# Optimization experiments

Measured on AMD Instinct MI355X. Metric: run time of the kernel, lower is better.

Reference implementation:

```python
import jax, jax.numpy as jnp
import numpy as np

N_NODES = 100000
N_GRAPHS = 64
NEG_SLOPE = 0.2  # PyG GATConv default leaky_relu slope


def gat_conv(x, src, dst, W, a_src, a_dst, b, heads, out_c, concat, num_nodes):
    # x: [N, F_in]; W: [heads*out_c, F_in]; a_src/a_dst: [heads, out_c]
    h = (x @ W.T).reshape(num_nodes, heads, out_c)            # [N, H, C]
    s_src = jnp.sum(h * a_src, axis=-1)                       # [N, H]
    s_dst = jnp.sum(h * a_dst, axis=-1)                       # [N, H]
    e = jax.nn.leaky_relu(s_src[src] + s_dst[dst], NEG_SLOPE)  # [E, H]
    # segment softmax over incoming edges of each destination node
    m = jax.ops.segment_max(e, dst, num_segments=num_nodes)   # [N, H]
    m = jnp.where(jnp.isfinite(m), m, 0.0)
    e = jnp.exp(e - m[dst])
    denom = jax.ops.segment_sum(e, dst, num_segments=num_nodes)  # [N, H]
    alpha = e / (denom[dst] + 1e-16)                           # [E, H]
    msg = alpha[:, :, None] * h[src]                           # [E, H, C]
    out = jax.ops.segment_sum(msg, dst, num_segments=num_nodes)  # [N, H, C]
    if concat:
        out = out.reshape(num_nodes, heads * out_c)
    else:
        out = out.mean(axis=1)
    return out + b


def setup_inputs() -> dict:
    key = jax.random.key(0)
    ks = jax.random.split(key, 12)
    x = jax.random.normal(ks[0], (N_NODES, 128), dtype=jnp.float32)
    edge_index = jax.random.randint(ks[1], (2, 1600000), 0, N_NODES, dtype=jnp.int64)
    batch = jnp.sort(jax.random.randint(ks[2], (N_NODES,), 0, N_GRAPHS, dtype=jnp.int64))
    # conv1: 128 -> 16, heads=4, concat -> 64
    W1 = jax.random.normal(ks[3], (64, 128), dtype=jnp.float32) * 0.1
    att_src1 = jax.random.normal(ks[4], (4, 16), dtype=jnp.float32) * 0.1
    att_dst1 = jax.random.normal(ks[5], (4, 16), dtype=jnp.float32) * 0.1
    b1 = jnp.zeros((64,), dtype=jnp.float32)
    # conv2: 64 -> 10, heads=1, concat=False
    W2 = jax.random.normal(ks[6], (10, 64), dtype=jnp.float32) * 0.1
    att_src2 = jax.random.normal(ks[7], (1, 10), dtype=jnp.float32) * 0.1
    att_dst2 = jax.random.normal(ks[8], (1, 10), dtype=jnp.float32) * 0.1
    b2 = jnp.zeros((10,), dtype=jnp.float32)
    return {"x": x, "edge_index": edge_index, "batch": batch,
            "W1": W1, "att_src1": att_src1, "att_dst1": att_dst1, "b1": b1,
            "W2": W2, "att_src2": att_src2, "att_dst2": att_dst2, "b2": b2}


def reference(x, edge_index, batch, W1, att_src1, att_dst1, b1, W2, att_src2, att_dst2, b2):
    N = x.shape[0]
    # PyG GATConv adds self-loops by default
    loop = jnp.arange(N, dtype=edge_index.dtype)
    src = jnp.concatenate([edge_index[0], loop])
    dst = jnp.concatenate([edge_index[1], loop])
    # dropout layers are inactive in eval mode
    h = gat_conv(x, src, dst, W1, att_src1, att_dst1, b1, heads=4, out_c=16, concat=True, num_nodes=N)
    h = jax.nn.elu(h)
    h = gat_conv(h, src, dst, W2, att_src2, att_dst2, b2, heads=1, out_c=10, concat=False, num_nodes=N)
    # global_mean_pool over graphs in the batch
    sums = jax.ops.segment_sum(h, batch, num_segments=N_GRAPHS)
    counts = jax.ops.segment_sum(jnp.ones((N,), dtype=h.dtype), batch, num_segments=N_GRAPHS)
    pooled = sums / jnp.maximum(counts, 1.0)[:, None]
    return jax.nn.log_softmax(pooled, axis=1)
```

## Files before the change

kernel.cpp:

```cpp
#include <hip/hip_runtime.h>
#include <hip/hip_bf16.h>
#include <math.h>

#define BSHIFT 7
#define BWIDTH (1 << BSHIFT)
#define BCAP 2560
#define A3_TILE 4096

typedef float floatx2 __attribute__((ext_vector_type(2)));
typedef __attribute__((ext_vector_type(8))) short bf16x8;
typedef __attribute__((ext_vector_type(4))) float f32x4;

__device__ inline unsigned int f2bf(float f) {
    unsigned int u = __float_as_uint(f);
    return (u + 0x7FFFu + ((u >> 16) & 1u)) >> 16;
}
__device__ inline float bflo(unsigned int u) { return __uint_as_float(u << 16); }
__device__ inline float bfhi(unsigned int u) { return __uint_as_float(u & 0xFFFF0000u); }

__device__ inline void fp8x16_fma2(uint4 Wv, float we, floatx2* q) {
    floatx2 w2; w2[0] = we; w2[1] = we;
    q[0] += w2 * __builtin_amdgcn_cvt_pk_f32_fp8((int)Wv.x, false);
    q[1] += w2 * __builtin_amdgcn_cvt_pk_f32_fp8((int)Wv.x, true);
    q[2] += w2 * __builtin_amdgcn_cvt_pk_f32_fp8((int)Wv.y, false);
    q[3] += w2 * __builtin_amdgcn_cvt_pk_f32_fp8((int)Wv.y, true);
    q[4] += w2 * __builtin_amdgcn_cvt_pk_f32_fp8((int)Wv.z, false);
    q[5] += w2 * __builtin_amdgcn_cvt_pk_f32_fp8((int)Wv.z, true);
    q[6] += w2 * __builtin_amdgcn_cvt_pk_f32_fp8((int)Wv.w, false);
    q[7] += w2 * __builtin_amdgcn_cvt_pk_f32_fp8((int)Wv.w, true);
}

#define G1_BM 128

__device__ void gemm1_body(char* smem, int bid,
    const float* __restrict__ x, const float* __restrict__ W1,
    const float* __restrict__ a_src, const float* __restrict__ a_dst,
    unsigned char* __restrict__ h1f, float* __restrict__ s1s,
    float* __restrict__ s1d, int N)
{
    unsigned short (*xb)[136] = (unsigned short(*)[136])smem;
    unsigned short (*wb)[136] = (unsigned short(*)[136])(smem + 34816);
    float (*hls)[68] = (float(*)[68])smem;

    int tid = threadIdx.x;
    int nb = bid * G1_BM;

    #pragma unroll
    for (int r = 0; r < 8; ++r) {
        int i = tid + r * 256;
        int ch = i >> 5, kq = i & 31;
        float4 v = *(const float4*)&W1[ch * 128 + kq * 4];
        uint2 pk;
        pk.x = f2bf(v.x) | (f2bf(v.y) << 16);
        pk.y = f2bf(v.z) | (f2bf(v.w) << 16);
        *(uint2*)&wb[ch][kq * 4] = pk;
    }
    #pragma unroll
    for (int r = 0; r < 16; ++r) {
        int i = tid + r * 256;
        int nl = i >> 5, kq = i & 31;
        int n = nb + nl;
        float4 v = (n < N) ? *(const float4*)&x[(size_t)n * 128 + kq * 4]
                           : make_float4(0.f, 0.f, 0.f, 0.f);
        uint2 pk;
        pk.x = f2bf(v.x) | (f2bf(v.y) << 16);
        pk.y = f2bf(v.z) | (f2bf(v.w) << 16);
        *(uint2*)&xb[nl][kq * 4] = pk;
    }
    __syncthreads();

    int lane = tid & 63, wv = tid >> 6;
    int lr = lane & 15, lk = lane >> 4;
    f32x4 acc[2][4];
    #pragma unroll
    for (int mt = 0; mt < 2; ++mt)
        #pragma unroll
        for (int nt = 0; nt < 4; ++nt) acc[mt][nt] = (f32x4){0.f, 0.f, 0.f, 0.f};

    #pragma unroll
    for (int ks = 0; ks < 4; ++ks) {
        int k0 = ks * 32 + lk * 8;
        bf16x8 af0 = *(const bf16x8*)&xb[wv * 32 + lr][k0];
        bf16x8 af1 = *(const bf16x8*)&xb[wv * 32 + 16 + lr][k0];
        #pragma unroll
        for (int nt = 0; nt < 4; ++nt) {
            bf16x8 bf = *(const bf16x8*)&wb[nt * 16 + lr][k0];
            acc[0][nt] = __builtin_amdgcn_mfma_f32_16x16x32_bf16(af0, bf, acc[0][nt], 0, 0, 0);
            acc[1][nt] = __builtin_amdgcn_mfma_f32_16x16x32_bf16(af1, bf, acc[1][nt], 0, 0, 0);
        }
    }
    __syncthreads();
    #pragma unroll
    for (int mt = 0; mt < 2; ++mt)
        #pragma unroll
        for (int nt = 0; nt < 4; ++nt)
            #pragma unroll
            for (int reg = 0; reg < 4; ++reg)
                hls[wv * 32 + mt * 16 + lk * 4 + reg][nt * 16 + lr] = acc[mt][nt][reg];
    __syncthreads();

    int nl = tid >> 1, half = tid & 1;
    int n = nb + nl;
    if (n < N) {
        float v[32];
        #pragma unroll
        for (int q = 0; q < 8; ++q) {
            float4 t4 = *(const float4*)&hls[nl][half * 32 + q * 4];
            v[q*4+0] = t4.x; v[q*4+1] = t4.y; v[q*4+2] = t4.z; v[q*4+3] = t4.w;
        }
        int h0 = half * 2, h1 = half * 2 + 1;
        float ss0 = 0.f, sd0 = 0.f, ss1 = 0.f, sd1 = 0.f;
        #pragma unroll
        for (int j = 0; j < 16; ++j) {
            ss0 += v[j] * a_src[h0 * 16 + j];
            sd0 += v[j] * a_dst[h0 * 16 + j];
            ss1 += v[16 + j] * a_src[h1 * 16 + j];
            sd1 += v[16 + j] * a_dst[h1 * 16 + j];
        }
        s1s[n * 4 + h0] = ss0; s1d[n * 4 + h0] = sd0;
        s1s[n * 4 + h1] = ss1; s1d[n * 4 + h1] = sd1;

        unsigned int w0, w1v, w2v, w3v, w4v, w5v, w6v, w7v;
        w0  = (unsigned)__builtin_amdgcn_cvt_pk_fp8_f32(v[0],  v[1],  0, false);
        w0  = (unsigned)__builtin_amdgcn_cvt_pk_fp8_f32(v[2],  v[3],  (int)w0, true);
        w1v = (unsigned)__builtin_amdgcn_cvt_pk_fp8_f32(v[4],  v[5],  0, false);
        w1v = (unsigned)__builtin_amdgcn_cvt_pk_fp8_f32(v[6],  v[7],  (int)w1v, true);
        w2v = (unsigned)__builtin_amdgcn_cvt_pk_fp8_f32(v[8],  v[9],  0, false);
        w2v = (unsigned)__builtin_amdgcn_cvt_pk_fp8_f32(v[10], v[11], (int)w2v, true);
        w3v = (unsigned)__builtin_amdgcn_cvt_pk_fp8_f32(v[12], v[13], 0, false);
        w3v = (unsigned)__builtin_amdgcn_cvt_pk_fp8_f32(v[14], v[15], (int)w3v, true);
        w4v = (unsigned)__builtin_amdgcn_cvt_pk_fp8_f32(v[16], v[17], 0, false);
        w4v = (unsigned)__builtin_amdgcn_cvt_pk_fp8_f32(v[18], v[19], (int)w4v, true);
        w5v = (unsigned)__builtin_amdgcn_cvt_pk_fp8_f32(v[20], v[21], 0, false);
        w5v = (unsigned)__builtin_amdgcn_cvt_pk_fp8_f32(v[22], v[23], (int)w5v, true);
        w6v = (unsigned)__builtin_amdgcn_cvt_pk_fp8_f32(v[24], v[25], 0, false);
        w6v = (unsigned)__builtin_amdgcn_cvt_pk_fp8_f32(v[26], v[27], (int)w6v, true);
        w7v = (unsigned)__builtin_amdgcn_cvt_pk_fp8_f32(v[28], v[29], 0, false);
        w7v = (unsigned)__builtin_amdgcn_cvt_pk_fp8_f32(v[30], v[31], (int)w7v, true);
        *(uint4*)(h1f + (size_t)n * 64 + half * 32)      = make_uint4(w0, w1v, w2v, w3v);
        *(uint4*)(h1f + (size_t)n * 64 + half * 32 + 16) = make_uint4(w4v, w5v, w6v, w7v);
    }
}

__device__ void partition_body(char* smem, int bid,
    const int* __restrict__ ei, int* __restrict__ bcnt, int* __restrict__ pairs,
    int E, int NBK)
{
    int* hist       = (int*)smem;
    int* scanb      = hist + 1024;
    int* gbase      = scanb + 1024;
    int* partial    = gbase + 1024;
    int* stage_pack = partial + 256;
    int* stage_pos  = stage_pack + A3_TILE;

    int t = threadIdx.x;
    int e0 = bid * A3_TILE;
    for (int i = t; i < 1024; i += 256) hist[i] = 0;
    __syncthreads();
    int my_b[16], my_rank[16], my_pack[16];
    #pragma unroll
    for (int j = 0; j < 16; ++j) {
        int e = e0 + j * 256 + t;
        int b = -1, pack = 0, r = 0;
        if (e < E) {
            int s = ei[e], d = ei[E + e];
            b = d >> BSHIFT;
            pack = ((d & (BWIDTH - 1)) << 17) | s;
            r = atomicAdd(&hist[b], 1);
        }
        my_b[j] = b; my_pack[j] = pack; my_rank[j] = r;
    }
    __syncthreads();
    int b4 = t * 4;
    int h0 = hist[b4], h1v = hist[b4 + 1], h2v = hist[b4 + 2], h3v = hist[b4 + 3];
    int tot = h0 + h1v + h2v + h3v;
    partial[t] = tot;
    __syncthreads();
    for (int o = 1; o < 256; o <<= 1) {
        int u = (t >= o) ? partial[t - o] : 0;
        __syncthreads();
        partial[t] += u;
        __syncthreads();
    }
    int excl = partial[t] - tot;
    scanb[b4]     = excl;
    scanb[b4 + 1] = excl + h0;
    scanb[b4 + 2] = excl + h0 + h1v;
    scanb[b4 + 3] = excl + h0 + h1v + h2v;
    int nvalid = partial[255];
    for (int b = t; b < NBK; b += 256) {
        int c = hist[b];
        if (c > 0) gbase[b] = b * BCAP + atomicAdd(&bcnt[b], c);
    }
    __syncthreads();
    #pragma unroll
    for (int j = 0; j < 16; ++j) {
        int b = my_b[j];
        if (b >= 0) {
            int slot = scanb[b] + my_rank[j];
            stage_pack[slot] = my_pack[j];
            stage_pos[slot]  = gbase[b] + my_rank[j];
        }
    }
    __syncthreads();
    for (int i = t; i < nvalid; i += 256)
        pairs[stage_pos[i]] = stage_pack[i];
}

__global__ __launch_bounds__(256) void gp_kernel(
    const float* __restrict__ x, const float* __restrict__ W1,
    const float* __restrict__ a_src, const float* __restrict__ a_dst,
    unsigned char* __restrict__ h1f, float* __restrict__ s1s,
    float* __restrict__ s1d, const int* __restrict__ ei,
    int* __restrict__ bcnt, int* __restrict__ pairs,
    int N, int E, int NBK, int G1B)
{
    __shared__ __align__(16) char smem[52224];
    if ((int)blockIdx.x < G1B)
        gemm1_body(smem, blockIdx.x, x, W1, a_src, a_dst, h1f, s1s, s1d, N);
    else
        partition_body(smem, blockIdx.x - G1B, ei, bcnt, pairs, E, NBK);
}

__global__ __launch_bounds__(256) void buildcsr_kernel(
    const int* __restrict__ pairs, const int* __restrict__ bcnt,
    int* __restrict__ csr_src, int* __restrict__ meta, int N)
{
    int b = blockIdx.x;
    __shared__ int stage[BCAP];
    __shared__ int hist[BWIDTH];
    __shared__ int scn[BWIDTH];
    __shared__ int cur[BWIDTH];
    int t = threadIdx.x;
    if (t < BWIDTH) hist[t] = 0;
    __syncthreads();
    int cnt = bcnt[b];
    int base = b * BCAP;
    for (int i = t; i < cnt; i += 256) {
        int p = pairs[base + i];
        stage[i] = p;
        atomicAdd(&hist[(p >> 17) & (BWIDTH - 1)], 1);
    }
    __syncthreads();
    int v = (t < BWIDTH) ? hist[t] : 0;
    if (t < BWIDTH) scn[t] = v;
    __syncthreads();
    for (int o = 1; o < BWIDTH; o <<= 1) {
        int u = (t < BWIDTH && t >= o) ? scn[t - o] : 0;
        __syncthreads();
        if (t < BWIDTH) scn[t] += u;
        __syncthreads();
    }
    if (t < BWIDTH) {
        int excl = scn[t] - v;
        cur[t] = excl;
        int dst = b * BWIDTH + t;
        if (dst < N) meta[dst] = (excl << 16) | v;
    }
    __syncthreads();
    for (int i = t; i < cnt; i += 256) {
        int p = stage[i];
        int slot = atomicAdd(&cur[(p >> 17) & (BWIDTH - 1)], 1);
        csr_src[base + slot] = p & 0x1FFFF;
    }
}

__global__ __launch_bounds__(256) void agg1_kernel(
    const int* __restrict__ meta, const int* __restrict__ csr_src,
    const unsigned char* __restrict__ h1f, const float* __restrict__ s1s,
    const float* __restrict__ s1d, const float* __restrict__ b1,
    const float* __restrict__ W2, const float* __restrict__ as2,
    const float* __restrict__ ad2, unsigned short* __restrict__ h2p, int N)
{
    __shared__ float w2s[640];
    for (int i = threadIdx.x; i < 640; i += 256) w2s[i] = W2[i];
    __syncthreads();

    int tid = blockIdx.x * 256 + threadIdx.x;
    int n = tid >> 4, h = tid & 3, sub = (tid >> 2) & 3;
    floatx2 xq[8];
    #pragma unroll
    for (int j = 0; j < 8; ++j) { xq[j][0] = 0.f; xq[j][1] = 0.f; }
    float den = 0.f;

    if (n < N) {
        float sdst = s1d[n * 4 + h];
        if (sub == 0) {
            float s = s1s[n * 4 + h] + sdst;
            s = (s >= 0.f) ? s : 0.2f * s;
            float w = __expf(s);
            den = w;
            uint4 Wv = *(const uint4*)(h1f + ((size_t)n << 6) + (h << 4));
            fp8x16_fma2(Wv, w, xq);
        }
        int mn = meta[n];
        int row = (n >> BSHIFT) * BCAP + (mn >> 16);
        int end = row + (mn & 0xFFFF);
        int i = row + sub;
        for (; i + 4 < end; i += 8) {
            int src0 = csr_src[i];
            int src1 = csr_src[i + 4];
            uint4 W0 = *(const uint4*)(h1f + ((size_t)src0 << 6) + (h << 4));
            uint4 W1 = *(const uint4*)(h1f + ((size_t)src1 << 6) + (h << 4));
            float a0 = s1s[src0 * 4 + h];
            float a1 = s1s[src1 * 4 + h];
            float e0 = a0 + sdst; e0 = (e0 >= 0.f) ? e0 : 0.2f * e0;
            float e1 = a1 + sdst; e1 = (e1 >= 0.f) ? e1 : 0.2f * e1;
            float w0 = __expf(e0);
            float w1 = __expf(e1);
            den += w0 + w1;
            fp8x16_fma2(W0, w0, xq);
            fp8x16_fma2(W1, w1, xq);
        }
        if (i < end) {
            int src = csr_src[i];
            uint4 Wv = *(const uint4*)(h1f + ((size_t)src << 6) + (h << 4));
            float ss = s1s[src * 4 + h] + sdst;
            ss = (ss >= 0.f) ? ss : 0.2f * ss;
            float we = __expf(ss);
            den += we;
            fp8x16_fma2(Wv, we, xq);
        }
    }
    float* xl = (float*)xq;
    #pragma unroll
    for (int j = 0; j < 16; ++j) {
        xl[j] += __shfl_xor(xl[j], 4);
        xl[j] += __shfl_xor(xl[j], 8);
    }
    den += __shfl_xor(den, 4);
    den += __shfl_xor(den, 8);

    float inv = 1.f / (den + 1e-16f);
    #pragma unroll
    for (int j = 0; j < 16; ++j) {
        float v = xl[j] * inv + b1[h * 16 + j];
        xl[j] = (v > 0.f) ? v : (__expf(v) - 1.f);
    }

    int clo = sub * 3;
    int nc = (sub == 3) ? 1 : 3;
    float part[3] = {0.f, 0.f, 0.f};
    #pragma unroll
    for (int idx = 0; idx < 3; ++idx) {
        if (idx < nc) {
            const float* wr = &w2s[(clo + idx) * 64 + h * 16];
            float p = 0.f;
            #pragma unroll
            for (int j = 0; j < 16; ++j) p += xl[j] * wr[j];
            part[idx] = p;
        }
    }
    #pragma unroll
    for (int idx = 0; idx < 3; ++idx) {
        part[idx] += __shfl_xor(part[idx], 1);
        part[idx] += __shfl_xor(part[idx], 2);
    }
    float ssp = 0.f, sdp = 0.f;
    #pragma unroll
    for (int idx = 0; idx < 3; ++idx) {
        if (idx < nc) {
            ssp += part[idx] * as2[clo + idx];
            sdp += part[idx] * ad2[clo + idx];
        }
    }
    ssp += __shfl_xor(ssp, 4); ssp += __shfl_xor(ssp, 8);
    sdp += __shfl_xor(sdp, 4); sdp += __shfl_xor(sdp, 8);

    if (n < N && h == 0) {
        #pragma unroll
        for (int idx = 0; idx < 3; ++idx)
            if (idx < nc)
                h2p[(size_t)n * 16 + clo + idx] = (unsigned short)f2bf(part[idx]);
        if (sub == 3) {
            h2p[(size_t)n * 16 + 10] = (unsigned short)f2bf(ssp);
            h2p[(size_t)n * 16 + 11] = (unsigned short)f2bf(sdp);
        }
    }
}

__global__ __launch_bounds__(256) void agg2_kernel(
    const int* __restrict__ meta, const int* __restrict__ csr_src,
    const unsigned short* __restrict__ h2p, const float* __restrict__ b2,
    float* __restrict__ node_out, int N)
{
    int tid = blockIdx.x * 256 + threadIdx.x;
    int n = tid >> 3, t = tid & 7;
    if (n >= N) return;
    floatx2 aq[5];
    #pragma unroll
    for (int c = 0; c < 5; ++c) { aq[c][0] = 0.f; aq[c][1] = 0.f; }
    float den = 0.f;

    uint2 d1 = *(const uint2*)(h2p + (size_t)n * 16 + 8);
    float sdst = bfhi(d1.y);
    if (t == 0) {
        uint4 d0 = *(const uint4*)(h2p + (size_t)n * 16);
        float s = bflo(d1.y) + sdst;
        s = (s >= 0.f) ? s : 0.2f * s;
        float w = __expf(s);
        den = w;
        floatx2 w2; w2[0] = w; w2[1] = w;
        floatx2 p;
        p[0] = bflo(d0.x); p[1] = bfhi(d0.x); aq[0] += w2 * p;
        p[0] = bflo(d0.y); p[1] = bfhi(d0.y); aq[1] += w2 * p;
        p[0] = bflo(d0.z); p[1] = bfhi(d0.z); aq[2] += w2 * p;
        p[0] = bflo(d0.w); p[1] = bfhi(d0.w); aq[3] += w2 * p;
        p[0] = bflo(d1.x); p[1] = bfhi(d1.x); aq[4] += w2 * p;
    }
    int mn = meta[n];
    int row = (n >> BSHIFT) * BCAP + (mn >> 16);
    int end = row + (mn & 0xFFFF);
    int i = row + t;
    for (; i + 8 < end; i += 16) {
        int src0 = csr_src[i];
        int src1 = csr_src[i + 8];
        uint4 A0 = *(const uint4*)(h2p + (size_t)src0 * 16);
        uint2 B0 = *(const uint2*)(h2p + (size_t)src0 * 16 + 8);
        uint4 A1 = *(const uint4*)(h2p + (size_t)src1 * 16);
        uint2 B1 = *(const uint2*)(h2p + (size_t)src1 * 16 + 8);
        float e0 = bflo(B0.y) + sdst; e0 = (e0 >= 0.f) ? e0 : 0.2f * e0;
        float e1 = bflo(B1.y) + sdst; e1 = (e1 >= 0.f) ? e1 : 0.2f * e1;
        float w0 = __expf(e0);
        float w1 = __expf(e1);
        den += w0 + w1;
        floatx2 w20; w20[0] = w0; w20[1] = w0;
        floatx2 w21; w21[0] = w1; w21[1] = w1;
        floatx2 p;
        p[0] = bflo(A0.x); p[1] = bfhi(A0.x); aq[0] += w20 * p;
        p[0] = bflo(A0.y); p[1] = bfhi(A0.y); aq[1] += w20 * p;
        p[0] = bflo(A0.z); p[1] = bfhi(A0.z); aq[2] += w20 * p;
        p[0] = bflo(A0.w); p[1] = bfhi(A0.w); aq[3] += w20 * p;
        p[0] = bflo(B0.x); p[1] = bfhi(B0.x); aq[4] += w20 * p;
        p[0] = bflo(A1.x); p[1] = bfhi(A1.x); aq[0] += w21 * p;
        p[0] = bflo(A1.y); p[1] = bfhi(A1.y); aq[1] += w21 * p;
        p[0] = bflo(A1.z); p[1] = bfhi(A1.z); aq[2] += w21 * p;
        p[0] = bflo(A1.w); p[1] = bfhi(A1.w); aq[3] += w21 * p;
        p[0] = bflo(B1.x); p[1] = bfhi(B1.x); aq[4] += w21 * p;
    }
    if (i < end) {
        int src = csr_src[i];
        uint4 A0 = *(const uint4*)(h2p + (size_t)src * 16);
        uint2 B0 = *(const uint2*)(h2p + (size_t)src * 16 + 8);
        float s = bflo(B0.y) + sdst;
        s = (s >= 0.f) ? s : 0.2f * s;
        float we = __expf(s);
        den += we;
        floatx2 w2; w2[0] = we; w2[1] = we;
        floatx2 p;
        p[0] = bflo(A0.x); p[1] = bfhi(A0.x); aq[0] += w2 * p;
        p[0] = bflo(A0.y); p[1] = bfhi(A0.y); aq[1] += w2 * p;
        p[0] = bflo(A0.z); p[1] = bfhi(A0.z); aq[2] += w2 * p;
        p[0] = bflo(A0.w); p[1] = bfhi(A0.w); aq[3] += w2 * p;
        p[0] = bflo(B0.x); p[1] = bfhi(B0.x); aq[4] += w2 * p;
    }
    float* acc = (float*)aq;
    #pragma unroll
    for (int c = 0; c < 10; ++c) {
        acc[c] += __shfl_xor(acc[c], 1);
        acc[c] += __shfl_xor(acc[c], 2);
        acc[c] += __shfl_xor(acc[c], 4);
    }
    den += __shfl_xor(den, 1);
    den += __shfl_xor(den, 2);
    den += __shfl_xor(den, 4);

    if (t == 0) {
        float inv = 1.f / (den + 1e-16f);
        float* o = &node_out[(size_t)n * 12];
        *(float4*)o = make_float4(acc[0]*inv + b2[0], acc[1]*inv + b2[1],
                                  acc[2]*inv + b2[2], acc[3]*inv + b2[3]);
        *(float4*)(o + 4) = make_float4(acc[4]*inv + b2[4], acc[5]*inv + b2[5],
                                        acc[6]*inv + b2[6], acc[7]*inv + b2[7]);
        *(float2*)(o + 8) = make_float2(acc[8]*inv + b2[8], acc[9]*inv + b2[9]);
    }
}

__global__ __launch_bounds__(256) void pool_kernel(
    const float* __restrict__ node_out, const int* __restrict__ batch,
    float* __restrict__ pooled, float* __restrict__ cnt, int N)
{
    int g = blockIdx.x;
    int lo = 0, hi = N;
    while (lo < hi) { int m = (lo + hi) >> 1; if (batch[m] < g) lo = m + 1; else hi = m; }
    int s0 = lo;
    hi = N;
    while (lo < hi) { int m = (lo + hi) >> 1; if (batch[m] < g + 1) lo = m + 1; else hi = m; }
    int s1 = lo;

    float acc[10];
    #pragma unroll
    for (int c = 0; c < 10; ++c) acc[c] = 0.f;
    for (int i = s0 + threadIdx.x; i < s1; i += 256) {
        const float* o = &node_out[(size_t)i * 12];
        float4 a = *(const float4*)o;
        float4 b = *(const float4*)(o + 4);
        float2 d = *(const float2*)(o + 8);
        acc[0] += a.x; acc[1] += a.y; acc[2] += a.z; acc[3] += a.w;
        acc[4] += b.x; acc[5] += b.y; acc[6] += b.z; acc[7] += b.w;
        acc[8] += d.x; acc[9] += d.y;
    }
    #pragma unroll
    for (int c = 0; c < 10; ++c)
        for (int o = 32; o > 0; o >>= 1) acc[c] += __shfl_down(acc[c], o);
    __shared__ float part[4][10];
    int wave = threadIdx.x >> 6, lane = threadIdx.x & 63;
    if (lane == 0)
        #pragma unroll
        for (int c = 0; c < 10; ++c) part[wave][c] = acc[c];
    __syncthreads();
    if (threadIdx.x < 10) {
        float s = part[0][threadIdx.x] + part[1][threadIdx.x]
                + part[2][threadIdx.x] + part[3][threadIdx.x];
        pooled[g * 10 + threadIdx.x] = s;
        if (threadIdx.x == 0) cnt[g] = (float)(s1 - s0);
    }
}

__global__ void final_kernel(const float* __restrict__ pooled,
                             const float* __restrict__ cnt, float* __restrict__ out)
{
    int g = threadIdx.x;
    if (g >= 64) return;
    float c = cnt[g];
    if (c < 1.f) c = 1.f;
    float v[10], m = -1e30f;
    #pragma unroll
    for (int i = 0; i < 10; ++i) {
        v[i] = pooled[g * 10 + i] / c;
        m = fmaxf(m, v[i]);
    }
    float s = 0.f;
    #pragma unroll
    for (int i = 0; i < 10; ++i) s += __expf(v[i] - m);
    float lse = m + logf(s);
    #pragma unroll
    for (int i = 0; i < 10; ++i) out[g * 10 + i] = v[i] - lse;
}

extern "C" void kernel_launch(void* const* d_in, const int* in_sizes, int n_in,
                              void* d_out, int out_size, void* d_ws, size_t ws_size,
                              hipStream_t stream) {
    const float* x       = (const float*)d_in[0];
    const int*   ei      = (const int*)  d_in[1];
    const int*   batch   = (const int*)  d_in[2];
    const float* W1      = (const float*)d_in[3];
    const float* a_src1  = (const float*)d_in[4];
    const float* a_dst1  = (const float*)d_in[5];
    const float* b1      = (const float*)d_in[6];
    const float* W2      = (const float*)d_in[7];
    const float* a_src2  = (const float*)d_in[8];
    const float* a_dst2  = (const float*)d_in[9];
    const float* b2      = (const float*)d_in[10];
    float* out = (float*)d_out;

    int N = in_sizes[0] / 128;
    int E = in_sizes[1] / 2;
    int NBK = (N + BWIDTH - 1) >> BSHIFT;

    float* f = (float*)d_ws;
    size_t off = 0;
    unsigned char* h1f = (unsigned char*)(f + off);
    float* node_out = (float*)h1f;
    off += (size_t)N * 16;
    float* s1s  = f + off; off += (size_t)N * 4;
    float* s1d  = f + off; off += (size_t)N * 4;
    unsigned short* h2p = (unsigned short*)(f + off);
    int*  pairs = (int*)(f + off);
    size_t r1 = ((size_t)N * 8 > (size_t)NBK * BCAP) ? (size_t)N * 8 : (size_t)NBK * BCAP;
    off += r1;
    int* iw = (int*)(f + off);
    size_t ioff = 0;
    int* meta    = iw + ioff; ioff += (size_t)N;
    int* csr_src = iw + ioff; ioff += (size_t)NBK * BCAP;
    int* bcnt    = iw + ioff; ioff += (size_t)NBK;
    float* pooled = (float*)(iw + ioff);
    float* cnt    = pooled + 640;

    hipMemsetAsync((void*)bcnt, 0, (size_t)NBK * sizeof(int), stream);

    int g1_blocks = (N + G1_BM - 1) / G1_BM;
    int ntiles = (E + A3_TILE - 1) / A3_TILE;
    gp_kernel<<<g1_blocks + ntiles, 256, 0, stream>>>(
        x, W1, a_src1, a_dst1, h1f, s1s, s1d, ei, bcnt, pairs, N, E, NBK, g1_blocks);

    buildcsr_kernel<<<NBK, 256, 0, stream>>>(pairs, bcnt, csr_src, meta, N);

    agg1_kernel<<<(N * 16 + 255) / 256, 256, 0, stream>>>(
        meta, csr_src, h1f, s1s, s1d, b1, W2, a_src2, a_dst2, h2p, N);

    agg2_kernel<<<(N * 8 + 255) / 256, 256, 0, stream>>>(
        meta, csr_src, h2p, b2, node_out, N);

    pool_kernel<<<64, 256, 0, stream>>>(node_out, batch, pooled, cnt, N);

    final_kernel<<<1, 64, 0, stream>>>(pooled, cnt, out);
}
```

Baseline: 124.8 us.

## Precompute bf16 W1, hold B fragments in registers, shrink partition tile and LDS

A small setup kernel now converts W1 to bf16 once and zeroes the bucket counters, replacing the memset. The GEMM blocks load their W1 MFMA fragments straight into registers instead of staging them in shared memory. The edge partition tile is halved to 2048, which lets the fused kernel's LDS shrink from about 52 KB to about 34 KB, with a launch-bounds hint for 4 blocks per SIMD-group. The aim is higher occupancy and less per-block conversion work. In exchange it adds an extra launch, more register pressure from the 16 held fragments, and twice as many partition blocks doing global bucket atomics.

```diff
diff --git a/kernel.cpp b/kernel.cpp
--- a/kernel.cpp
+++ b/kernel.cpp
@@ -5,7 +5,7 @@
 #define BSHIFT 7
 #define BWIDTH (1 << BSHIFT)
 #define BCAP 2560
-#define A3_TILE 4096
+#define A3_TILE 2048
 
 typedef float floatx2 __attribute__((ext_vector_type(2)));
 typedef __attribute__((ext_vector_type(8))) short bf16x8;
@@ -32,29 +32,48 @@
 
 #define G1_BM 128
 
+__global__ __launch_bounds__(256) void setup_kernel(
+    int* __restrict__ bcnt, int NBK,
+    const float* __restrict__ W1, unsigned short* __restrict__ w1b)
+{
+    if (blockIdx.x == 0) {
+        for (int i = threadIdx.x; i < NBK; i += 256) bcnt[i] = 0;
+    } else {
+        int t = threadIdx.x;
+        #pragma unroll
+        for (int r = 0; r < 8; ++r) {
+            int i4 = t + r * 256;
+            int ch = i4 >> 5, kq = i4 & 31;
+            float4 v = *(const float4*)&W1[ch * 128 + kq * 4];
+            uint2 pk;
+            pk.x = f2bf(v.x) | (f2bf(v.y) << 16);
+            pk.y = f2bf(v.z) | (f2bf(v.w) << 16);
+            *(uint2*)&w1b[ch * 128 + kq * 4] = pk;
+        }
+    }
+}
+
 __device__ void gemm1_body(char* smem, int bid,
-    const float* __restrict__ x, const float* __restrict__ W1,
+    const float* __restrict__ x, const unsigned short* __restrict__ w1b,
     const float* __restrict__ a_src, const float* __restrict__ a_dst,
     unsigned char* __restrict__ h1f, float* __restrict__ s1s,
     float* __restrict__ s1d, int N)
 {
     unsigned short (*xb)[136] = (unsigned short(*)[136])smem;
-    unsigned short (*wb)[136] = (unsigned short(*)[136])(smem + 34816);
     float (*hls)[68] = (float(*)[68])smem;
 
     int tid = threadIdx.x;
     int nb = bid * G1_BM;
-
-    #pragma unroll
-    for (int r = 0; r < 8; ++r) {
-        int i = tid + r * 256;
-        int ch = i >> 5, kq = i & 31;
-        float4 v = *(const float4*)&W1[ch * 128 + kq * 4];
-        uint2 pk;
-        pk.x = f2bf(v.x) | (f2bf(v.y) << 16);
-        pk.y = f2bf(v.z) | (f2bf(v.w) << 16);
-        *(uint2*)&wb[ch][kq * 4] = pk;
-    }
+    int lane = tid & 63, wv = tid >> 6;
+    int lr = lane & 15, lk = lane >> 4;
+
+    bf16x8 Bf[4][4];
+    #pragma unroll
+    for (int ks = 0; ks < 4; ++ks)
+        #pragma unroll
+        for (int nt = 0; nt < 4; ++nt)
+            Bf[ks][nt] = *(const bf16x8*)&w1b[(nt * 16 + lr) * 128 + ks * 32 + lk * 8];
+
     #pragma unroll
     for (int r = 0; r < 16; ++r) {
         int i = tid + r * 256;
@@ -69,8 +88,6 @@
     }
     __syncthreads();
 
-    int lane = tid & 63, wv = tid >> 6;
-    int lr = lane & 15, lk = lane >> 4;
     f32x4 acc[2][4];
     #pragma unroll
     for (int mt = 0; mt < 2; ++mt)
@@ -84,9 +101,8 @@
         bf16x8 af1 = *(const bf16x8*)&xb[wv * 32 + 16 + lr][k0];
         #pragma unroll
         for (int nt = 0; nt < 4; ++nt) {
-            bf16x8 bf = *(const bf16x8*)&wb[nt * 16 + lr][k0];
-            acc[0][nt] = __builtin_amdgcn_mfma_f32_16x16x32_bf16(af0, bf, acc[0][nt], 0, 0, 0);
-            acc[1][nt] = __builtin_amdgcn_mfma_f32_16x16x32_bf16(af1, bf, acc[1][nt], 0, 0, 0);
+            acc[0][nt] = __builtin_amdgcn_mfma_f32_16x16x32_bf16(af0, Bf[ks][nt], acc[0][nt], 0, 0, 0);
+            acc[1][nt] = __builtin_amdgcn_mfma_f32_16x16x32_bf16(af1, Bf[ks][nt], acc[1][nt], 0, 0, 0);
         }
     }
     __syncthreads();
@@ -157,9 +173,9 @@
     int e0 = bid * A3_TILE;
     for (int i = t; i < 1024; i += 256) hist[i] = 0;
     __syncthreads();
-    int my_b[16], my_rank[16], my_pack[16];
-    #pragma unroll
-    for (int j = 0; j < 16; ++j) {
+    int my_b[8], my_rank[8], my_pack[8];
+    #pragma unroll
+    for (int j = 0; j < 8; ++j) {
         int e = e0 + j * 256 + t;
         int b = -1, pack = 0, r = 0;
         if (e < E) {
@@ -194,7 +210,7 @@
     }
     __syncthreads();
     #pragma unroll
-    for (int j = 0; j < 16; ++j) {
+    for (int j = 0; j < 8; ++j) {
         int b = my_b[j];
         if (b >= 0) {
             int slot = scanb[b] + my_rank[j];
@@ -207,17 +223,17 @@
         pairs[stage_pos[i]] = stage_pack[i];
 }
 
-__global__ __launch_bounds__(256) void gp_kernel(
-    const float* __restrict__ x, const float* __restrict__ W1,
+__global__ __launch_bounds__(256, 4) void gp_kernel(
+    const float* __restrict__ x, const unsigned short* __restrict__ w1b,
     const float* __restrict__ a_src, const float* __restrict__ a_dst,
     unsigned char* __restrict__ h1f, float* __restrict__ s1s,
     float* __restrict__ s1d, const int* __restrict__ ei,
     int* __restrict__ bcnt, int* __restrict__ pairs,
     int N, int E, int NBK, int G1B)
 {
-    __shared__ __align__(16) char smem[52224];
+    __shared__ __align__(16) char smem[34816];
     if ((int)blockIdx.x < G1B)
-        gemm1_body(smem, blockIdx.x, x, W1, a_src, a_dst, h1f, s1s, s1d, N);
+        gemm1_body(smem, blockIdx.x, x, w1b, a_src, a_dst, h1f, s1s, s1d, N);
     else
         partition_body(smem, blockIdx.x - G1B, ei, bcnt, pairs, E, NBK);
 }
@@ -565,6 +581,7 @@
     off += (size_t)N * 16;
     float* s1s  = f + off; off += (size_t)N * 4;
     float* s1d  = f + off; off += (size_t)N * 4;
+    unsigned short* w1b = (unsigned short*)(f + off); off += 4096;
     unsigned short* h2p = (unsigned short*)(f + off);
     int*  pairs = (int*)(f + off);
     size_t r1 = ((size_t)N * 8 > (size_t)NBK * BCAP) ? (size_t)N * 8 : (size_t)NBK * BCAP;
@@ -577,12 +594,13 @@
     float* pooled = (float*)(iw + ioff);
     float* cnt    = pooled + 640;
 
-    hipMemsetAsync((void*)bcnt, 0, (size_t)NBK * sizeof(int), stream);
-
     int g1_blocks = (N + G1_BM - 1) / G1_BM;
     int ntiles = (E + A3_TILE - 1) / A3_TILE;
+
+    setup_kernel<<<2, 256, 0, stream>>>(bcnt, NBK, W1, w1b);
+
     gp_kernel<<<g1_blocks + ntiles, 256, 0, stream>>>(
-        x, W1, a_src1, a_dst1, h1f, s1s, s1d, ei, bcnt, pairs, N, E, NBK, g1_blocks);
+        x, w1b, a_src1, a_dst1, h1f, s1s, s1d, ei, bcnt, pairs, N, E, NBK, g1_blocks);
 
     buildcsr_kernel<<<NBK, 256, 0, stream>>>(pairs, bcnt, csr_src, meta, N);
 
```

New measurement: 129.7 us. +3.9%, slower.
